# Kernel optimization log

Hardware: AMD Instinct MI355X
Metric: run time of the kernel (lower is better)

Reference implementation:

```python
import jax, jax.numpy as jnp
import numpy as np

DIM = 2048
N_HEAD = 16

def setup_inputs() -> dict:
    key = jax.random.key(0)
    ks = jax.random.split(key, 5)
    s_in = 1.0 / np.sqrt(DIM)
    x = jax.random.normal(ks[0], (4, 2048, DIM), dtype=jnp.float32)
    W_attn = jax.random.normal(ks[1], (DIM, 3 * DIM), dtype=jnp.float32) * s_in
    b_attn = jnp.zeros((3 * DIM,), dtype=jnp.float32)
    W_proj = jax.random.normal(ks[2], (DIM, DIM), dtype=jnp.float32) * s_in
    b_proj = jnp.zeros((DIM,), dtype=jnp.float32)
    return {"x": x, "W_attn": W_attn, "b_attn": b_attn, "W_proj": W_proj, "b_proj": b_proj}

def reference(x, W_attn, b_attn, W_proj, b_proj):
    B, T, C = x.shape
    H = N_HEAD
    Dh = C // H
    qkv = x @ W_attn + b_attn              # [B,T,3C]
    q, k, v = jnp.split(qkv, 3, axis=-1)
    # [B,T,C] -> [B,H,T,Dh]
    q = q.reshape(B, T, H, Dh).transpose(0, 2, 1, 3)
    k = k.reshape(B, T, H, Dh).transpose(0, 2, 1, 3)
    v = v.reshape(B, T, H, Dh).transpose(0, 2, 1, 3)
    scale = 1.0 / jnp.sqrt(jnp.asarray(Dh, dtype=x.dtype))
    att = jnp.einsum('bhqd,bhkd->bhqk', q, k) * scale
    att = jax.nn.softmax(att, axis=-1)
    y = jnp.einsum('bhqk,bhkd->bhqd', att, v)  # [B,H,T,Dh]
    y = y.transpose(0, 2, 1, 3).reshape(B, T, C)
    y = y @ W_proj + b_proj
    return y
```

## Files before the change

kernel.cpp:

```cpp
#include <hip/hip_runtime.h>


using bhalf  = __bf16;
using bhalf8 = __attribute__((ext_vector_type(8))) __bf16;
using floatx4 = __attribute__((ext_vector_type(4))) float;

#define MFMA16(A, B, C) __builtin_amdgcn_mfma_f32_16x16x32_bf16(A, B, C, 0, 0, 0)

__device__ __forceinline__ void gload16(const void* g, void* l) {
  __builtin_amdgcn_global_load_lds(
      (const __attribute__((address_space(1))) unsigned int*)g,
      (__attribute__((address_space(3))) unsigned int*)l, 16, 0, 0);
}

constexpr int Bn = 4, Tn = 2048, Cn = 2048, Hn = 16, Dh = 128;
constexpr int Kdim = Cn;
constexpr size_t SLOT = (size_t)Hn * Tn * Dh;

__global__ __launch_bounds__(256) void cvt_x(const float* __restrict__ in,
                                             bhalf* __restrict__ out) {
  const size_t i = ((size_t)blockIdx.x * 256 + threadIdx.x) * 8;
  const float4 a = *reinterpret_cast<const float4*>(in + i);
  const float4 b = *reinterpret_cast<const float4*>(in + i + 4);
  bhalf8 v;
  v[0] = (bhalf)a.x; v[1] = (bhalf)a.y; v[2] = (bhalf)a.z; v[3] = (bhalf)a.w;
  v[4] = (bhalf)b.x; v[5] = (bhalf)b.y; v[6] = (bhalf)b.z; v[7] = (bhalf)b.w;
  *reinterpret_cast<bhalf8*>(out + i) = v;
}

__global__ __launch_bounds__(256) void transpose_cvt(const float* __restrict__ in,
                                                     bhalf* __restrict__ out,
                                                     int ldin, int ldout, int coff) {
  __shared__ unsigned short tile[64][65];
  const int c0 = blockIdx.x * 64, r0 = blockIdx.y * 64;
  const int tx = threadIdx.x & 15, ty = threadIdx.x >> 4;
#pragma unroll
  for (int i = 0; i < 4; i++) {
    const int r = ty + i * 16;
    const float4 u = *reinterpret_cast<const float4*>(in + (size_t)(r0 + r) * ldin + coff + c0 + tx * 4);
    tile[r][tx * 4 + 0] = __builtin_bit_cast(unsigned short, (bhalf)u.x);
    tile[r][tx * 4 + 1] = __builtin_bit_cast(unsigned short, (bhalf)u.y);
    tile[r][tx * 4 + 2] = __builtin_bit_cast(unsigned short, (bhalf)u.z);
    tile[r][tx * 4 + 3] = __builtin_bit_cast(unsigned short, (bhalf)u.w);
  }
  __syncthreads();
#pragma unroll
  for (int i = 0; i < 4; i++) {
    const int c = ty + i * 16;
    ushort4 u;
    u.x = tile[tx * 4 + 0][c]; u.y = tile[tx * 4 + 1][c];
    u.z = tile[tx * 4 + 2][c]; u.w = tile[tx * 4 + 3][c];
    *reinterpret_cast<ushort4*>((unsigned short*)out + (size_t)(c0 + c) * ldout + r0 + tx * 4) = u;
  }
}

__global__ __launch_bounds__(256, 3) void gemm_qk(const bhalf* __restrict__ A,
                                                  const bhalf* __restrict__ Bt,
                                                  const float* __restrict__ bias,
                                                  bhalf* __restrict__ oq,
                                                  bhalf* __restrict__ ok) {
  __shared__ __align__(16) bhalf sA[128 * 64];
  __shared__ __align__(16) bhalf sB[128 * 64];
  const int tid = threadIdx.x;
  const int lane = tid & 63, wv = tid >> 6;
  const int ln = lane & 15, quad = lane >> 4;
  const int wr = wv >> 1, wc = wv & 1;
  const int m0 = blockIdx.y * 128, n0 = blockIdx.x * 128;

  const floatx4 fzero = {0.f, 0.f, 0.f, 0.f};
  floatx4 acc[4][4];
#pragma unroll
  for (int i = 0; i < 4; i++)
#pragma unroll
    for (int j = 0; j < 4; j++) acc[i][j] = fzero;

  const int schunk = (lane & 7) ^ ((lane >> 3) & 7);
  const bhalf* aStage = A + (size_t)(m0 + wv * 32 + (lane >> 3)) * Kdim + schunk * 8;
  const bhalf* bStage = Bt + (size_t)(n0 + wv * 32 + (lane >> 3)) * Kdim + schunk * 8;
  bhalf* sAw = &sA[(wv * 32) * 64];
  bhalf* sBw = &sB[(wv * 32) * 64];

  for (int k0 = 0; k0 < Kdim; k0 += 64) {
#pragma unroll
    for (int j = 0; j < 4; j++) gload16(aStage + (size_t)j * 8 * Kdim + k0, sAw + j * 8 * 64);
#pragma unroll
    for (int j = 0; j < 4; j++) gload16(bStage + (size_t)j * 8 * Kdim + k0, sBw + j * 8 * 64);
    __syncthreads();
#pragma unroll
    for (int ks = 0; ks < 2; ks++) {
      bhalf8 af[4], bfr[4];
#pragma unroll
      for (int mi = 0; mi < 4; mi++)
        af[mi] = *reinterpret_cast<const bhalf8*>(
            &sA[(wr * 64 + mi * 16 + ln) * 64 + ((ks * 4 + quad) ^ (ln & 7)) * 8]);
#pragma unroll
      for (int ni = 0; ni < 4; ni++)
        bfr[ni] = *reinterpret_cast<const bhalf8*>(
            &sB[(wc * 64 + ni * 16 + ln) * 64 + ((ks * 4 + quad) ^ (ln & 7)) * 8]);
#pragma unroll
      for (int mi = 0; mi < 4; mi++)
#pragma unroll
        for (int ni = 0; ni < 4; ni++)
          acc[mi][ni] = MFMA16(af[mi], bfr[ni], acc[mi][ni]);
    }
    __syncthreads();
  }

  const int b = m0 >> 11, t0 = m0 & 2047;
  const int which = n0 >> 11;
  const int h = (n0 & 2047) >> 7;
  bhalf* op = which == 0 ? oq : ok;
  float bv[4];
#pragma unroll
  for (int ni = 0; ni < 4; ni++) bv[ni] = bias[n0 + wc * 64 + ni * 16 + ln];
  const size_t base = (size_t)b * (2 * SLOT) + ((size_t)h * Tn + t0) * Dh;
#pragma unroll
  for (int mi = 0; mi < 4; mi++)
#pragma unroll
    for (int ni = 0; ni < 4; ni++)
#pragma unroll
      for (int r = 0; r < 4; r++) {
        const int t = wr * 64 + mi * 16 + quad * 4 + r;
        const int d = wc * 64 + ni * 16 + ln;
        op[base + (size_t)t * Dh + d] = (bhalf)(acc[mi][ni][r] + bv[ni]);
      }
}

template <int MODE>
__global__ __launch_bounds__(256, 3) void gemm_xa(const float* __restrict__ A,
                                                  const bhalf* __restrict__ Bt,
                                                  const float* __restrict__ bias,
                                                  bhalf* __restrict__ oq,
                                                  bhalf* __restrict__ ok) {
  __shared__ __align__(16) float sA[128 * 64];
  __shared__ __align__(16) bhalf sB[128 * 64];
  const int tid = threadIdx.x;
  const int lane = tid & 63, wv = tid >> 6;
  const int ln = lane & 15, quad = lane >> 4;
  const int wr = wv >> 1, wc = wv & 1;
  const int m0 = blockIdx.y * 128, n0 = blockIdx.x * 128;

  const floatx4 fzero = {0.f, 0.f, 0.f, 0.f};
  floatx4 acc[4][4];
#pragma unroll
  for (int i = 0; i < 4; i++)
#pragma unroll
    for (int j = 0; j < 4; j++) acc[i][j] = fzero;

  const int schunkB = (lane & 7) ^ ((lane >> 3) & 7);
  const bhalf* bStage = Bt + (size_t)(n0 + wv * 32 + (lane >> 3)) * Kdim + schunkB * 8;
  bhalf* sBw = &sB[(wv * 32) * 64];
  const int rA = lane >> 4, cA = lane & 15;
  float* sAw = &sA[(wv * 32) * 64];

  for (int k0 = 0; k0 < Kdim; k0 += 64) {
#pragma unroll
    for (int j = 0; j < 8; j++) {
      const int rloc = j * 4 + rA;
      const int gc = cA ^ (rloc & 15);
      gload16(A + (size_t)(m0 + wv * 32 + rloc) * Kdim + k0 + gc * 4, sAw + (j * 4) * 64);
    }
#pragma unroll
    for (int j = 0; j < 4; j++) gload16(bStage + (size_t)j * 8 * Kdim + k0, sBw + j * 8 * 64);
    __syncthreads();
#pragma unroll
    for (int ks = 0; ks < 2; ks++) {
      bhalf8 af[4], bfr[4];
#pragma unroll
      for (int mi = 0; mi < 4; mi++) {
        const int row = wr * 64 + mi * 16 + ln;
        const int c0c = ks * 8 + quad * 2;
        const float4 lo = *reinterpret_cast<const float4*>(&sA[row * 64 + ((c0c ^ ln) * 4)]);
        const float4 hi = *reinterpret_cast<const float4*>(&sA[row * 64 + (((c0c + 1) ^ ln) * 4)]);
        bhalf8 t;
        t[0] = (bhalf)lo.x; t[1] = (bhalf)lo.y; t[2] = (bhalf)lo.z; t[3] = (bhalf)lo.w;
        t[4] = (bhalf)hi.x; t[5] = (bhalf)hi.y; t[6] = (bhalf)hi.z; t[7] = (bhalf)hi.w;
        af[mi] = t;
      }
#pragma unroll
      for (int ni = 0; ni < 4; ni++)
        bfr[ni] = *reinterpret_cast<const bhalf8*>(
            &sB[(wc * 64 + ni * 16 + ln) * 64 + ((ks * 4 + quad) ^ (ln & 7)) * 8]);
#pragma unroll
      for (int i = 0; i < 4; i++)
#pragma unroll
        for (int j = 0; j < 4; j++) {
          if (MODE == 2)
            acc[i][j] = MFMA16(bfr[i], af[j], acc[i][j]);
          else
            acc[i][j] = MFMA16(af[i], bfr[j], acc[i][j]);
        }
    }
    __syncthreads();
  }

  const int b = m0 >> 11, t0 = m0 & 2047;
  if (MODE == 0) {
    const int which = n0 >> 11;
    const int h = (n0 & 2047) >> 7;
    bhalf* op = which == 0 ? oq : ok;
    float bv[4];
#pragma unroll
    for (int ni = 0; ni < 4; ni++) bv[ni] = bias[n0 + wc * 64 + ni * 16 + ln];
    const size_t base = (size_t)b * (2 * SLOT) + ((size_t)h * Tn + t0) * Dh;
#pragma unroll
    for (int mi = 0; mi < 4; mi++)
#pragma unroll
      for (int ni = 0; ni < 4; ni++)
#pragma unroll
        for (int r = 0; r < 4; r++) {
          const int t = wr * 64 + mi * 16 + quad * 4 + r;
          const int d = wc * 64 + ni * 16 + ln;
          op[base + (size_t)t * Dh + d] = (bhalf)(acc[mi][ni][r] + bv[ni]);
        }
  } else {
    const int h = n0 >> 7;
    const size_t base = (size_t)(b * Hn + h) * Dh * Tn;
#pragma unroll
    for (int ni = 0; ni < 4; ni++)
#pragma unroll
      for (int mi = 0; mi < 4; mi++)
#pragma unroll
        for (int r = 0; r < 4; r++) {
          const int d = wc * 64 + ni * 16 + quad * 4 + r;
          const int t = t0 + wr * 64 + mi * 16 + ln;
          oq[base + (size_t)d * Tn + t] = (bhalf)(acc[ni][mi][r] + bias[n0 + d]);
        }
  }
}

__global__ __launch_bounds__(256, 3) void gemm_proj(const bhalf* __restrict__ A,
                                                    const bhalf* __restrict__ Bt,
                                                    const float* __restrict__ bias,
                                                    float* __restrict__ of) {
  __shared__ __align__(16) bhalf sA[128 * 64];
  __shared__ __align__(16) bhalf sB[128 * 64];
  const int tid = threadIdx.x;
  const int lane = tid & 63, wv = tid >> 6;
  const int ln = lane & 15, quad = lane >> 4;
  const int wr = wv >> 1, wc = wv & 1;
  const int m0 = blockIdx.y * 128, n0 = blockIdx.x * 128;

  const floatx4 fzero = {0.f, 0.f, 0.f, 0.f};
  floatx4 acc[4][4];
#pragma unroll
  for (int i = 0; i < 4; i++)
#pragma unroll
    for (int j = 0; j < 4; j++) acc[i][j] = fzero;

  const int schunk = (lane & 7) ^ ((lane >> 3) & 7);
  const bhalf* aStage = A + (size_t)(m0 + wv * 32 + (lane >> 3)) * Kdim + schunk * 8;
  const bhalf* bStage = Bt + (size_t)(n0 + wv * 32 + (lane >> 3)) * Kdim + schunk * 8;
  bhalf* sAw = &sA[(wv * 32) * 64];
  bhalf* sBw = &sB[(wv * 32) * 64];

  for (int k0 = 0; k0 < Kdim; k0 += 64) {
#pragma unroll
    for (int j = 0; j < 4; j++) gload16(aStage + (size_t)j * 8 * Kdim + k0, sAw + j * 8 * 64);
#pragma unroll
    for (int j = 0; j < 4; j++) gload16(bStage + (size_t)j * 8 * Kdim + k0, sBw + j * 8 * 64);
    __syncthreads();
#pragma unroll
    for (int ks = 0; ks < 2; ks++) {
      bhalf8 af[4], bfr[4];
#pragma unroll
      for (int mi = 0; mi < 4; mi++)
        af[mi] = *reinterpret_cast<const bhalf8*>(
            &sA[(wr * 64 + mi * 16 + ln) * 64 + ((ks * 4 + quad) ^ (ln & 7)) * 8]);
#pragma unroll
      for (int ni = 0; ni < 4; ni++)
        bfr[ni] = *reinterpret_cast<const bhalf8*>(
            &sB[(wc * 64 + ni * 16 + ln) * 64 + ((ks * 4 + quad) ^ (ln & 7)) * 8]);
#pragma unroll
      for (int mi = 0; mi < 4; mi++)
#pragma unroll
        for (int ni = 0; ni < 4; ni++)
          acc[mi][ni] = MFMA16(af[mi], bfr[ni], acc[mi][ni]);
    }
    __syncthreads();
  }

  float bv[4];
#pragma unroll
  for (int ni = 0; ni < 4; ni++) bv[ni] = bias[n0 + wc * 64 + ni * 16 + ln];
#pragma unroll
  for (int mi = 0; mi < 4; mi++)
#pragma unroll
    for (int ni = 0; ni < 4; ni++)
#pragma unroll
      for (int r = 0; r < 4; r++) {
        const int row = m0 + wr * 64 + mi * 16 + quad * 4 + r;
        const int col = n0 + wc * 64 + ni * 16 + ln;
        of[(size_t)row * Cn + col] = acc[mi][ni][r] + bv[ni];
      }
}

__global__ __launch_bounds__(256, 2) void flash_attn_k(const bhalf* __restrict__ Qb,
                                                       const bhalf* __restrict__ Kb,
                                                       const bhalf* __restrict__ VTb,
                                                       bhalf* __restrict__ Ob) {
  __shared__ __align__(16) bhalf sK[128 * 128];
  __shared__ __align__(16) bhalf sVT[128 * 128];
  const int tid = threadIdx.x;
  const int lane = tid & 63, wv = tid >> 6;
  const int ln = lane & 15, quad = lane >> 4;
  const int rl = lane >> 4, cl = lane & 15;
  const int l = blockIdx.x + (int)gridDim.x * blockIdx.y;
  const int h = ((l & 7) << 1) | ((l >> 3) & 1);
  const int t0q = (l >> 4) * 64;
  const size_t hb = (size_t)h * Tn * Dh;
  constexpr float kSc = 0.08838834764831845f * 1.4426950408889634f;

  bhalf8 qf[4];
#pragma unroll
  for (int kd = 0; kd < 4; kd++)
    qf[kd] = *reinterpret_cast<const bhalf8*>(
        Qb + hb + (size_t)(t0q + wv * 16 + ln) * Dh + kd * 32 + quad * 8);

  const floatx4 fzero = {0.f, 0.f, 0.f, 0.f};
  floatx4 oAcc[8];
#pragma unroll
  for (int di = 0; di < 8; di++) oAcc[di] = fzero;
  float lrow[4] = {0.f, 0.f, 0.f, 0.f};

  for (int t0k = 0; t0k < Tn; t0k += 128) {
#pragma unroll
    for (int j = 0; j < 8; j++) {
      const int rloc = wv * 32 + j * 4 + rl;
      const int c = cl ^ (rloc & 15);
      gload16(Kb + hb + (size_t)(t0k + rloc) * Dh + c * 8, sK + (wv * 32 + j * 4) * 128);
    }
#pragma unroll
    for (int j = 0; j < 8; j++) {
      const int rloc = wv * 32 + j * 4 + rl;
      const int c = cl ^ (rloc & 15);
      gload16(VTb + hb + (size_t)rloc * Tn + t0k + c * 8, sVT + (wv * 32 + j * 4) * 128);
    }
    __syncthreads();

    floatx4 sAcc[8];
#pragma unroll
    for (int ni = 0; ni < 8; ni++) sAcc[ni] = fzero;
#pragma unroll
    for (int kd = 0; kd < 4; kd++) {
#pragma unroll
      for (int ni = 0; ni < 8; ni++) {
        const bhalf8 bfr = *reinterpret_cast<const bhalf8*>(
            &sK[(ni * 16 + ln) * 128 + ((kd * 4 + quad) ^ ln) * 8]);
        sAcc[ni] = MFMA16(qf[kd], bfr, sAcc[ni]);
      }
    }

#pragma unroll
    for (int r = 0; r < 4; r++) {
      float rs = 0.f;
#pragma unroll
      for (int ni = 0; ni < 8; ni++) {
        const float p = exp2f(sAcc[ni][r] * kSc);
        sAcc[ni][r] = p;
        rs += p;
      }
      rs += __shfl_xor(rs, 1);
      rs += __shfl_xor(rs, 2);
      rs += __shfl_xor(rs, 4);
      rs += __shfl_xor(rs, 8);
      lrow[r] += rs;
    }
    __syncthreads();

#pragma unroll
    for (int ni = 0; ni < 8; ni++)
#pragma unroll
      for (int r = 0; r < 4; r++) {
        const int qrow = wv * 16 + quad * 4 + r;
        const int kcol = ni * 16 + ln;
        sK[qrow * 128 + (((kcol >> 3) ^ (qrow & 15)) * 8) + (kcol & 7)] =
            (bhalf)sAcc[ni][r];
      }
    __syncthreads();

#pragma unroll
    for (int kt = 0; kt < 4; kt++) {
      const bhalf8 ap = *reinterpret_cast<const bhalf8*>(
          &sK[(wv * 16 + ln) * 128 + ((kt * 4 + quad) ^ ln) * 8]);
#pragma unroll
      for (int di = 0; di < 8; di++) {
        const bhalf8 bv = *reinterpret_cast<const bhalf8*>(
            &sVT[(di * 16 + ln) * 128 + ((kt * 4 + quad) ^ ln) * 8]);
        oAcc[di] = MFMA16(ap, bv, oAcc[di]);
      }
    }
    __syncthreads();
  }

#pragma unroll
  for (int r = 0; r < 4; r++) {
    const float inv = 1.0f / lrow[r];
    const int t = t0q + wv * 16 + quad * 4 + r;
    const size_t rowb = (size_t)t * Cn + h * Dh;
#pragma unroll
    for (int di = 0; di < 8; di++)
      Ob[rowb + di * 16 + ln] = (bhalf)(oAcc[di][r] * inv);
  }
}

extern "C" void kernel_launch(void* const* d_in, const int* in_sizes, int n_in,
                              void* d_out, int out_size, void* d_ws, size_t ws_size,
                              hipStream_t stream) {
  const float* x      = (const float*)d_in[0];
  const float* W_attn = (const float*)d_in[1];
  const float* b_attn = (const float*)d_in[2];
  const float* W_proj = (const float*)d_in[3];
  const float* b_proj = (const float*)d_in[4];
  float* out = (float*)d_out;
  bhalf* ws  = (bhalf*)d_ws;

  bhalf* xb   = ws;
  bhalf* wtQK = ws + 4 * SLOT;
  bhalf* wtV  = ws;
  bhalf* vt   = ws + 2 * SLOT;
  bhalf* y    = ws;
  bhalf* wtP  = ws + 4 * SLOT;
  bhalf* qk   = (bhalf*)d_out;

  cvt_x<<<8192, 256, 0, stream>>>(x, xb);

  transpose_cvt<<<dim3(64, 32), 256, 0, stream>>>(W_attn, wtQK, 3 * Cn, Kdim, 0);
  gemm_qk<<<dim3(32, 64), 256, 0, stream>>>(xb, wtQK, b_attn, qk, qk + SLOT);

  transpose_cvt<<<dim3(32, 32), 256, 0, stream>>>(W_attn, wtV, 3 * Cn, Kdim, 2 * Cn);
  gemm_xa<2><<<dim3(16, 64), 256, 0, stream>>>(x, wtV, b_attn + 2 * Cn, vt, nullptr);

  for (int b = 0; b < Bn; b++)
    flash_attn_k<<<dim3(32, 16), 256, 0, stream>>>(qk + (size_t)b * 2 * SLOT,
                                                   qk + (size_t)b * 2 * SLOT + SLOT,
                                                   vt + (size_t)b * SLOT,
                                                   y + (size_t)b * SLOT);

  transpose_cvt<<<dim3(32, 32), 256, 0, stream>>>(W_proj, wtP, Kdim, Kdim, 0);
  gemm_proj<<<dim3(16, 64), 256, 0, stream>>>(y, wtP, b_proj, out);
}
```

Before: 762.8 us.

## Pipeline K/V tile loads in flash attention and merge batch launches

The attention kernel now writes P to a separate LDS buffer, so the next K tile can be prefetched while P·V runs and the next V tile is fetched during the following QK step. Full syncthreads are replaced by explicit waitcnt plus barrier, and MFMA sections get raised wave priority. The four per-batch launches become one larger grid, and gemm_qk's occupancy hint rises from 3 to 4. The extra 16KB of LDS may limit occupancy, and the tighter register budget in gemm_qk could cause spills.

```diff
diff --git a/kernel.cpp b/kernel.cpp
--- a/kernel.cpp
+++ b/kernel.cpp
@@ -54,7 +54,7 @@
   }
 }
 
-__global__ __launch_bounds__(256, 3) void gemm_qk(const bhalf* __restrict__ A,
+__global__ __launch_bounds__(256, 4) void gemm_qk(const bhalf* __restrict__ A,
                                                   const bhalf* __restrict__ Bt,
                                                   const float* __restrict__ bias,
                                                   bhalf* __restrict__ oq,
@@ -295,19 +295,25 @@
       }
 }
 
-__global__ __launch_bounds__(256, 2) void flash_attn_k(const bhalf* __restrict__ Qb,
-                                                       const bhalf* __restrict__ Kb,
-                                                       const bhalf* __restrict__ VTb,
-                                                       bhalf* __restrict__ Ob) {
+__global__ __launch_bounds__(256, 2) void flash_attn_all(const bhalf* __restrict__ qk,
+                                                         const bhalf* __restrict__ vt,
+                                                         bhalf* __restrict__ yb) {
   __shared__ __align__(16) bhalf sK[128 * 128];
   __shared__ __align__(16) bhalf sVT[128 * 128];
+  __shared__ __align__(16) bhalf sP[64 * 128];
   const int tid = threadIdx.x;
   const int lane = tid & 63, wv = tid >> 6;
   const int ln = lane & 15, quad = lane >> 4;
   const int rl = lane >> 4, cl = lane & 15;
   const int l = blockIdx.x + (int)gridDim.x * blockIdx.y;
-  const int h = ((l & 7) << 1) | ((l >> 3) & 1);
-  const int t0q = (l >> 4) * 64;
+  const int b = l >> 9;
+  const int l5 = l & 511;
+  const int h = ((l5 & 7) << 1) | ((l5 >> 3) & 1);
+  const int t0q = (l5 >> 4) * 64;
+  const bhalf* Qb  = qk + (size_t)b * 2 * SLOT;
+  const bhalf* Kb  = Qb + SLOT;
+  const bhalf* VTb = vt + (size_t)b * SLOT;
+  bhalf* Ob        = yb + (size_t)b * SLOT;
   const size_t hb = (size_t)h * Tn * Dh;
   constexpr float kSc = 0.08838834764831845f * 1.4426950408889634f;
 
@@ -323,24 +329,36 @@
   for (int di = 0; di < 8; di++) oAcc[di] = fzero;
   float lrow[4] = {0.f, 0.f, 0.f, 0.f};
 
-  for (int t0k = 0; t0k < Tn; t0k += 128) {
+  auto stageK = [&](int t0k) {
 #pragma unroll
     for (int j = 0; j < 8; j++) {
       const int rloc = wv * 32 + j * 4 + rl;
       const int c = cl ^ (rloc & 15);
       gload16(Kb + hb + (size_t)(t0k + rloc) * Dh + c * 8, sK + (wv * 32 + j * 4) * 128);
     }
+  };
+  auto stageV = [&](int t0k) {
 #pragma unroll
     for (int j = 0; j < 8; j++) {
       const int rloc = wv * 32 + j * 4 + rl;
       const int c = cl ^ (rloc & 15);
       gload16(VTb + hb + (size_t)rloc * Tn + t0k + c * 8, sVT + (wv * 32 + j * 4) * 128);
     }
-    __syncthreads();
+  };
+
+  stageK(0);
+  asm volatile("" ::: "memory");
+  stageV(0);
+
+  for (int t0k = 0; t0k < Tn; t0k += 128) {
+    asm volatile("s_waitcnt vmcnt(8)" ::: "memory");
+    __builtin_amdgcn_s_barrier();
+    asm volatile("" ::: "memory");
 
     floatx4 sAcc[8];
 #pragma unroll
     for (int ni = 0; ni < 8; ni++) sAcc[ni] = fzero;
+    __builtin_amdgcn_s_setprio(1);
 #pragma unroll
     for (int kd = 0; kd < 4; kd++) {
 #pragma unroll
@@ -350,6 +368,7 @@
         sAcc[ni] = MFMA16(qf[kd], bfr, sAcc[ni]);
       }
     }
+    __builtin_amdgcn_s_setprio(0);
 
 #pragma unroll
     for (int r = 0; r < 4; r++) {
@@ -366,7 +385,11 @@
       rs += __shfl_xor(rs, 8);
       lrow[r] += rs;
     }
-    __syncthreads();
+
+    asm volatile("s_waitcnt vmcnt(0)" ::: "memory");
+    __builtin_amdgcn_s_barrier();
+    asm volatile("" ::: "memory");
+    if (t0k + 128 < Tn) stageK(t0k + 128);
 
 #pragma unroll
     for (int ni = 0; ni < 8; ni++)
@@ -374,15 +397,18 @@
       for (int r = 0; r < 4; r++) {
         const int qrow = wv * 16 + quad * 4 + r;
         const int kcol = ni * 16 + ln;
-        sK[qrow * 128 + (((kcol >> 3) ^ (qrow & 15)) * 8) + (kcol & 7)] =
+        sP[qrow * 128 + (((kcol >> 3) ^ (qrow & 15)) * 8) + (kcol & 7)] =
             (bhalf)sAcc[ni][r];
       }
-    __syncthreads();
-
+    asm volatile("s_waitcnt lgkmcnt(0)" ::: "memory");
+    __builtin_amdgcn_s_barrier();
+    asm volatile("" ::: "memory");
+
+    __builtin_amdgcn_s_setprio(1);
 #pragma unroll
     for (int kt = 0; kt < 4; kt++) {
       const bhalf8 ap = *reinterpret_cast<const bhalf8*>(
-          &sK[(wv * 16 + ln) * 128 + ((kt * 4 + quad) ^ ln) * 8]);
+          &sP[(wv * 16 + ln) * 128 + ((kt * 4 + quad) ^ ln) * 8]);
 #pragma unroll
       for (int di = 0; di < 8; di++) {
         const bhalf8 bv = *reinterpret_cast<const bhalf8*>(
@@ -390,7 +416,12 @@
         oAcc[di] = MFMA16(ap, bv, oAcc[di]);
       }
     }
-    __syncthreads();
+    __builtin_amdgcn_s_setprio(0);
+
+    asm volatile("s_waitcnt lgkmcnt(0)" ::: "memory");
+    __builtin_amdgcn_s_barrier();
+    asm volatile("" ::: "memory");
+    if (t0k + 128 < Tn) stageV(t0k + 128);
   }
 
 #pragma unroll
@@ -431,11 +462,7 @@
   transpose_cvt<<<dim3(32, 32), 256, 0, stream>>>(W_attn, wtV, 3 * Cn, Kdim, 2 * Cn);
   gemm_xa<2><<<dim3(16, 64), 256, 0, stream>>>(x, wtV, b_attn + 2 * Cn, vt, nullptr);
 
-  for (int b = 0; b < Bn; b++)
-    flash_attn_k<<<dim3(32, 16), 256, 0, stream>>>(qk + (size_t)b * 2 * SLOT,
-                                                   qk + (size_t)b * 2 * SLOT + SLOT,
-                                                   vt + (size_t)b * SLOT,
-                                                   y + (size_t)b * SLOT);
+  flash_attn_all<<<dim3(32, 64), 256, 0, stream>>>(qk, vt, y);
 
   transpose_cvt<<<dim3(32, 32), 256, 0, stream>>>(W_proj, wtP, Kdim, Kdim, 0);
   gemm_proj<<<dim3(16, 64), 256, 0, stream>>>(y, wtP, b_proj, out);
```

Result: faster. 712.5 us (-6.6%).
